# Optimization experiments

Hardware: AMD Instinct MI355X
Metric: run time of the kernel (lower is better)

## Reference

```python
import jax, jax.numpy as jnp
import numpy as np
from jax import lax

EPS = 1e-5

def _layernorm(x, g, b):
    m = x.mean(-1, keepdims=True)
    v = ((x - m) ** 2).mean(-1, keepdims=True)
    return (x - m) * lax.rsqrt(v + EPS) * g + b

def _batchnorm(x, g, b):
    # x: [N, C, L]; training-mode batch statistics (torch BatchNorm1d default)
    m = x.mean((0, 2), keepdims=True)
    v = ((x - m) ** 2).mean((0, 2), keepdims=True)
    return (x - m) * lax.rsqrt(v + EPS) * g[None, :, None] + b[None, :, None]

def _conv1d(x, w, bias, stride):
    y = lax.conv_general_dilated(x, w, window_strides=(stride,), padding='VALID',
                                 dimension_numbers=('NCH', 'OIH', 'NCH'))
    return y + bias[None, :, None]

def setup_inputs() -> dict:
    key = jax.random.key(0)
    ks = jax.random.split(key, 22)
    B, C, L = 512, 12, 5000
    NF, HID, LAT = 32, 64, 32
    def w(k, shape, fan_in):
        return jax.random.normal(k, shape, jnp.float32) * (1.0 / np.sqrt(fan_in))
    return {
        'x': jax.random.normal(ks[0], (B, C, L), jnp.float32),
        'c1w': w(ks[1], (32, C, 50), C * 50), 'c1b': jnp.zeros((32,), jnp.float32),
        'bn1g': jnp.ones((32,), jnp.float32), 'bn1b': jnp.zeros((32,), jnp.float32),
        'c2w': w(ks[2], (NF, 32, 25), 32 * 25), 'c2b': jnp.zeros((NF,), jnp.float32),
        'bn2g': jnp.ones((NF,), jnp.float32), 'bn2b': jnp.zeros((NF,), jnp.float32),
        'Wi': w(ks[3], (LAT, NF), NF) * 0.5, 'bi': jnp.zeros((LAT,), jnp.float32),
        'ln1g': jnp.ones((LAT,), jnp.float32), 'ln1b': jnp.zeros((LAT,), jnp.float32),
        'Wh': w(ks[4], (HID, LAT), LAT) * 0.5, 'bh': jnp.zeros((HID,), jnp.float32),
        'ln2g': jnp.ones((HID,), jnp.float32), 'ln2b': jnp.zeros((HID,), jnp.float32),
        'Wr': w(ks[5], (LAT, HID), HID) * 0.5, 'br': jnp.zeros((LAT,), jnp.float32),
        'Wo': w(ks[6], (LAT, LAT), LAT), 'bo': jnp.zeros((LAT,), jnp.float32),
    }

def reference(x, c1w, c1b, bn1g, bn1b, c2w, c2b, bn2g, bn2b,
              Wi, bi, ln1g, ln1b, Wh, bh, ln2g, ln2b, Wr, br, Wo, bo):
    # CNN front-end: [B,12,5000] -> [B,32,496] -> [B,32,95]
    h = jax.nn.relu(_batchnorm(_conv1d(x, c1w, c1b, 10), bn1g, bn1b))
    h = jax.nn.relu(_batchnorm(_conv1d(h, c2w, c2b, 5), bn2g, bn2b))
    feats = h.transpose(2, 0, 1)  # [T, B, NF]
    # input_proj + ln1 have no dependence on the recurrent state -> hoist out of loop
    xt_all = _layernorm(jnp.einsum('tbf,lf->tbl', feats, Wi) + bi, ln1g, ln1b)  # [T,B,LAT]

    def step(hstate, xt):
        combined = xt + hstate
        hp = jax.nn.relu(combined @ Wh.T + bh)      # [B, HID]
        hp = _layernorm(hp, ln2g, ln2b)
        hnew = jnp.tanh(hp @ Wr.T + br)             # [B, LAT]
        return hnew, hnew

    h0 = jnp.zeros((x.shape[0], Wr.shape[0]), x.dtype)
    _, outs = lax.scan(step, h0, xt_all)            # outs: [T, B, LAT]
    pooled = outs.mean(0)                           # mean over time
    return pooled @ Wo.T + bo                       # [B, LAT]
```

## Files before the change

kernel.cpp:

```cpp
#include <hip/hip_runtime.h>

#define EPS 1e-5f

#define B    512
#define C_IN 12
#define L_IN 5000
#define C1   32
#define L1   496
#define NF   32
#define L2   95
#define LAT  32
#define HID  64
#define T    L2

typedef short s16x8 __attribute__((ext_vector_type(8)));
typedef float f32x16 __attribute__((ext_vector_type(16)));

__device__ __forceinline__ ushort f2bf(float f) {
    uint u = __builtin_bit_cast(uint, f);
    u += 0x7fff + ((u >> 16) & 1);
    return (ushort)(u >> 16);
}
__device__ __forceinline__ float bf2f(ushort h) {
    return __builtin_bit_cast(float, (uint)h << 16);
}
__device__ __forceinline__ uint pk(float f) {
    ushort h = f2bf(f);
    return (uint)h | ((uint)f2bf(f - bf2f(h)) << 16);
}
__device__ __forceinline__ uint4 pack4(float4 d) {
    return make_uint4(pk(d.x), pk(d.y), pk(d.z), pk(d.w));
}

__global__ void k_prep_w(const float* __restrict__ c1w, const float* __restrict__ c2w,
                         ushort* __restrict__ wfrag1, ushort* __restrict__ wfrag2) {
    int i = blockIdx.x * 256 + threadIdx.x;
    if (i < 6144) {
        int lane = i & 63, r = i >> 6;
        int split = r & 1, s = (r >> 1) & 3, c = r >> 3;
        int oc = lane & 31, kbase = s * 16 + (lane >> 5) * 8;
        ushort o8[8];
#pragma unroll
        for (int j = 0; j < 8; ++j) {
            int kk = kbase + j;
            float w = (kk < 50) ? c1w[oc * 600 + c * 50 + kk] : 0.f;
            ushort hb = f2bf(w);
            o8[j] = split ? f2bf(w - bf2f(hb)) : hb;
        }
        ushort4* dst = reinterpret_cast<ushort4*>(wfrag1) + (size_t)i * 2;
        dst[0] = make_ushort4(o8[0], o8[1], o8[2], o8[3]);
        dst[1] = make_ushort4(o8[4], o8[5], o8[6], o8[7]);
    } else if (i < 14336) {
        int j = i - 6144;
        int lane = j & 63, r = j >> 6;
        int split = r & 1, ks = (r >> 1) & 1, c = r >> 2;
        int oc = lane & 31, kbase = ks * 16 + (lane >> 5) * 8;
        ushort o8[8];
#pragma unroll
        for (int jj = 0; jj < 8; ++jj) {
            int kk = kbase + jj;
            float w = (kk < 25) ? c2w[oc * 800 + c * 25 + kk] : 0.f;
            ushort hb = f2bf(w);
            o8[jj] = split ? f2bf(w - bf2f(hb)) : hb;
        }
        ushort4* dst = reinterpret_cast<ushort4*>(wfrag2) + (size_t)j * 2;
        dst[0] = make_ushort4(o8[0], o8[1], o8[2], o8[3]);
        dst[1] = make_ushort4(o8[4], o8[5], o8[6], o8[7]);
    }
}

__device__ __forceinline__ void conv1_compute(const uint (*xs)[1344], const uint4* wf4,
                                              int c0, int abase, int lane,
                                              f32x16& hh, f32x16& hl, f32x16& lh) {
    for (int cc = 0; cc < 6; ++cc) {
        const int c = c0 + cc;
        const uint* xc = xs[c];
        const uint4* wfc = wf4 + (size_t)c * 512 + lane;
#pragma unroll
        for (int s = 0; s < 4; ++s) {
            const int idx = abase + s * 16;
            uint2 p0 = *reinterpret_cast<const uint2*>(&xc[idx]);
            uint2 p1 = *reinterpret_cast<const uint2*>(&xc[idx + 2]);
            uint2 p2 = *reinterpret_cast<const uint2*>(&xc[idx + 4]);
            uint2 p3 = *reinterpret_cast<const uint2*>(&xc[idx + 6]);
            union { s16x8 v; uint u[4]; } ah, al, bh, bl;
            ah.u[0] = __builtin_amdgcn_perm(p0.y, p0.x, 0x05040100u);
            al.u[0] = __builtin_amdgcn_perm(p0.y, p0.x, 0x07060302u);
            ah.u[1] = __builtin_amdgcn_perm(p1.y, p1.x, 0x05040100u);
            al.u[1] = __builtin_amdgcn_perm(p1.y, p1.x, 0x07060302u);
            ah.u[2] = __builtin_amdgcn_perm(p2.y, p2.x, 0x05040100u);
            al.u[2] = __builtin_amdgcn_perm(p2.y, p2.x, 0x07060302u);
            ah.u[3] = __builtin_amdgcn_perm(p3.y, p3.x, 0x05040100u);
            al.u[3] = __builtin_amdgcn_perm(p3.y, p3.x, 0x07060302u);
            uint4 bq = wfc[s * 128];
            uint4 lq = wfc[s * 128 + 64];
            bh.u[0] = bq.x; bh.u[1] = bq.y; bh.u[2] = bq.z; bh.u[3] = bq.w;
            bl.u[0] = lq.x; bl.u[1] = lq.y; bl.u[2] = lq.z; bl.u[3] = lq.w;
            hh = __builtin_amdgcn_mfma_f32_32x32x16_bf16(ah.v, bh.v, hh, 0, 0, 0);
            hl = __builtin_amdgcn_mfma_f32_32x32x16_bf16(ah.v, bl.v, hl, 0, 0, 0);
            lh = __builtin_amdgcn_mfma_f32_32x32x16_bf16(al.v, bh.v, lh, 0, 0, 0);
        }
    }
}

__global__ __launch_bounds__(512, 4) void k_conv1(const float* __restrict__ x,
                                                  const ushort* __restrict__ wfrag,
                                                  const float* __restrict__ c1b,
                                                  float* __restrict__ y1,
                                                  float* __restrict__ raw1) {
    __shared__ uint xs[C_IN][1344];
    __shared__ float redS[4][32], redQ[4][32];
    const int chunk = blockIdx.x, b = blockIdx.y, tid = threadIdx.x;
    const int t0 = chunk * 128;
    const int v4max = min(336, (5000 - 10 * t0) >> 2);
    const float4* xb4 = reinterpret_cast<const float4*>(x + (size_t)b * (C_IN * L_IN) + 10 * t0);

    uint4* xs4 = reinterpret_cast<uint4*>(&xs[0][0]);
#pragma unroll
    for (int r = 0; r < 2; ++r) {
        float4 rg[4];
#pragma unroll
        for (int i = 0; i < 4; ++i) {
            const int v = tid + (r * 4 + i) * 512;
            const int c = v / 336, i4 = v - c * 336;
            rg[i] = make_float4(0, 0, 0, 0);
            if (v < 4032 && i4 < v4max) rg[i] = xb4[c * 1250 + i4];
        }
#pragma unroll
        for (int i = 0; i < 4; ++i) {
            const int v = tid + (r * 4 + i) * 512;
            if (v < 4032) xs4[v] = pack4(rg[i]);
        }
    }
    __syncthreads();

    const int lane = tid & 63, wv = tid >> 6;
    const int g = wv >> 2;
    const int tw = wv & 3;
    const int cl = lane & 31;
    const int kgrp = lane >> 5;
    const int abase = 10 * (tw * 32 + cl) + kgrp * 8;

    f32x16 hh, hl, lh;
#pragma unroll
    for (int i = 0; i < 16; ++i) { hh[i] = 0.f; hl[i] = 0.f; lh[i] = 0.f; }
    const uint4* wf4 = reinterpret_cast<const uint4*>(wfrag);

    conv1_compute(xs, wf4, g * 6, abase, lane, hh, hl, lh);

    f32x16 tot;
#pragma unroll
    for (int i = 0; i < 16; ++i) tot[i] = hh[i] + hl[i] + lh[i];

    __syncthreads();
    float4* pr = reinterpret_cast<float4*>(&xs[0][0]);
    if (g == 1) {
#pragma unroll
        for (int i4 = 0; i4 < 4; ++i4)
            pr[tw * 256 + i4 * 64 + lane] =
                make_float4(tot[4*i4], tot[4*i4+1], tot[4*i4+2], tot[4*i4+3]);
    }
    __syncthreads();

    float sum = 0.f, sq = 0.f;
    if (g == 0) {
        const float bias = c1b[cl];
        float* yb = y1 + ((size_t)b * C1 + cl) * L1;
#pragma unroll
        for (int q = 0; q < 4; ++q) {
            float4 p = pr[tw * 256 + q * 64 + lane];
            const int trow = t0 + tw * 32 + 8 * q + 4 * kgrp;
            float4 st;
            st.x = tot[4*q+0] + p.x + bias;
            st.y = tot[4*q+1] + p.y + bias;
            st.z = tot[4*q+2] + p.z + bias;
            st.w = tot[4*q+3] + p.w + bias;
            if (trow < L1) {
                *reinterpret_cast<float4*>(yb + trow) = st;
                sum += st.x + st.y + st.z + st.w;
                sq  += st.x * st.x + st.y * st.y + st.z * st.z + st.w * st.w;
            }
        }
        sum += __shfl_xor(sum, 32);
        sq  += __shfl_xor(sq, 32);
        if (lane < 32) { redS[tw][cl] = sum; redQ[tw][cl] = sq; }
    }
    __syncthreads();
    if (tid < 64) {
        int o = tid & 31, isQ = tid >> 5;
        float v = isQ ? (redQ[0][o] + redQ[1][o] + redQ[2][o] + redQ[3][o])
                      : (redS[0][o] + redS[1][o] + redS[2][o] + redS[3][o]);
        atomicAdd(&raw1[(isQ ? 1024 : 0) + o * 16], v);
    }
}

__global__ __launch_bounds__(384, 3) void k_conv2(const float* __restrict__ y1,
                                                  const ushort* __restrict__ wfrag2,
                                                  const float* __restrict__ c2b,
                                                  const float* __restrict__ raw1,
                                                  const float* __restrict__ bn1g,
                                                  const float* __restrict__ bn1b,
                                                  float* __restrict__ y2,
                                                  float* __restrict__ raw2) {
    __shared__ uint xs[C1 * 512];
    __shared__ float fin[64];
    __shared__ float redS[3][32], redQ[3][32];
    const int b = blockIdx.x, tid = threadIdx.x;

    if (tid < 32) {
        const float cnt = 1.f / (float)(B * L1);
        float mean = raw1[tid * 16] * cnt;
        float var = raw1[1024 + tid * 16] * cnt - mean * mean;
        float sc = bn1g[tid] * rsqrtf(var + EPS);
        fin[tid] = sc;
        fin[32 + tid] = bn1b[tid] - mean * sc;
    }
    __syncthreads();

    const float4* src = reinterpret_cast<const float4*>(y1 + (size_t)b * (C1 * L1));
    for (int v = tid; v < C1 * 128; v += 384) {
        const int c = v >> 7, i4 = v & 127;
        uint4 o = make_uint4(0, 0, 0, 0);
        if (i4 < 124) {
            const float sc = fin[c], sh = fin[32 + c];
            float4 d = src[c * 124 + i4];
            float e0 = fmaxf(fmaf(d.x, sc, sh), 0.f);
            float e1 = fmaxf(fmaf(d.y, sc, sh), 0.f);
            float e2 = fmaxf(fmaf(d.z, sc, sh), 0.f);
            float e3 = fmaxf(fmaf(d.w, sc, sh), 0.f);
            o = make_uint4(pk(e0), pk(e1), pk(e2), pk(e3));
        }
        *reinterpret_cast<uint4*>(&xs[c * 512 + 4 * i4]) = o;
    }
    __syncthreads();

    const int lane = tid & 63, wv = tid / 64;
    const int g = (wv >= 3) ? 1 : 0;
    const int tw = wv - 3 * g;
    const int cl = lane & 31;
    const int kgrp = lane >> 5;
    const int tbase = 5 * (tw * 32 + cl) + kgrp * 8;

    f32x16 hh, hl, lh;
#pragma unroll
    for (int i = 0; i < 16; ++i) { hh[i] = 0.f; hl[i] = 0.f; lh[i] = 0.f; }
    const uint4* wf4 = reinterpret_cast<const uint4*>(wfrag2);

    for (int cc = 0; cc < 16; ++cc) {
        const int c = g * 16 + cc;
        const uint* xc = xs + c * 512;
        const uint4* wfc = wf4 + (size_t)c * 256 + lane;
#pragma unroll
        for (int ks = 0; ks < 2; ++ks) {
            const int idx = tbase + ks * 16;
            uint u0 = xc[idx + 0], u1 = xc[idx + 1], u2 = xc[idx + 2], u3 = xc[idx + 3];
            uint u4 = xc[idx + 4], u5 = xc[idx + 5], u6 = xc[idx + 6], u7 = xc[idx + 7];
            union { s16x8 v; uint u[4]; } ah, al, bh, bl;
            ah.u[0] = __builtin_amdgcn_perm(u1, u0, 0x05040100u);
            al.u[0] = __builtin_amdgcn_perm(u1, u0, 0x07060302u);
            ah.u[1] = __builtin_amdgcn_perm(u3, u2, 0x05040100u);
            al.u[1] = __builtin_amdgcn_perm(u3, u2, 0x07060302u);
            ah.u[2] = __builtin_amdgcn_perm(u5, u4, 0x05040100u);
            al.u[2] = __builtin_amdgcn_perm(u5, u4, 0x07060302u);
            ah.u[3] = __builtin_amdgcn_perm(u7, u6, 0x05040100u);
            al.u[3] = __builtin_amdgcn_perm(u7, u6, 0x07060302u);
            uint4 bq = wfc[ks * 128];
            uint4 lq = wfc[ks * 128 + 64];
            bh.u[0] = bq.x; bh.u[1] = bq.y; bh.u[2] = bq.z; bh.u[3] = bq.w;
            bl.u[0] = lq.x; bl.u[1] = lq.y; bl.u[2] = lq.z; bl.u[3] = lq.w;
            hh = __builtin_amdgcn_mfma_f32_32x32x16_bf16(ah.v, bh.v, hh, 0, 0, 0);
            hl = __builtin_amdgcn_mfma_f32_32x32x16_bf16(ah.v, bl.v, hl, 0, 0, 0);
            lh = __builtin_amdgcn_mfma_f32_32x32x16_bf16(al.v, bh.v, lh, 0, 0, 0);
        }
    }

    f32x16 tot;
#pragma unroll
    for (int i = 0; i < 16; ++i) tot[i] = hh[i] + hl[i] + lh[i];

    __syncthreads();
    float4* pr = reinterpret_cast<float4*>(xs);
    if (g == 1) {
#pragma unroll
        for (int q = 0; q < 4; ++q)
            pr[tw * 256 + q * 64 + lane] =
                make_float4(tot[4*q], tot[4*q+1], tot[4*q+2], tot[4*q+3]);
    }
    __syncthreads();

    float sum = 0.f, sq = 0.f;
    if (g == 0) {
        const float bias = c2b[cl];
#pragma unroll
        for (int q = 0; q < 4; ++q) {
            float4 p = pr[tw * 256 + q * 64 + lane];
            float v4[4] = { tot[4*q+0] + p.x + bias, tot[4*q+1] + p.y + bias,
                            tot[4*q+2] + p.z + bias, tot[4*q+3] + p.w + bias };
#pragma unroll
            for (int j = 0; j < 4; ++j) {
                const int t = tw * 32 + 8 * q + 4 * kgrp + j;
                if (t < L2) {
                    y2[((size_t)b * L2 + t) * NF + cl] = v4[j];
                    sum += v4[j]; sq += v4[j] * v4[j];
                }
            }
        }
        sum += __shfl_xor(sum, 32);
        sq  += __shfl_xor(sq, 32);
        if (lane < 32) { redS[tw][cl] = sum; redQ[tw][cl] = sq; }
    }
    __syncthreads();
    if (tid < 64) {
        int o = tid & 31, isQ = tid >> 5;
        float v = isQ ? (redQ[0][o] + redQ[1][o] + redQ[2][o])
                      : (redS[0][o] + redS[1][o] + redS[2][o]);
        atomicAdd(&raw2[(isQ ? 1024 : 0) + o * 16], v);
    }
}

__global__ __launch_bounds__(256) void k_proj(const float* __restrict__ y2,
                                              const float* __restrict__ raw2,
                                              const float* __restrict__ bn2g,
                                              const float* __restrict__ bn2b,
                                              const float* __restrict__ Wi,
                                              const float* __restrict__ bi,
                                              const float* __restrict__ ln1g,
                                              const float* __restrict__ ln1b,
                                              const float* __restrict__ Wh,
                                              const float* __restrict__ bh,
                                              float* __restrict__ xt2) {
    __shared__ float fin[64];
    if (threadIdx.x < 32) {
        const float cnt = 1.f / (float)(B * L2);
        float mean = raw2[threadIdx.x * 16] * cnt;
        float var = raw2[1024 + threadIdx.x * 16] * cnt - mean * mean;
        float sc = bn2g[threadIdx.x] * rsqrtf(var + EPS);
        fin[threadIdx.x] = sc;
        fin[32 + threadIdx.x] = bn2b[threadIdx.x] - mean * sc;
    }
    __syncthreads();

    const int r = blockIdx.x * 256 + threadIdx.x;
    const int b = r / 95, t = r - b * 95;

    const float4* row = reinterpret_cast<const float4*>(y2 + (size_t)r * NF);
    float u[NF];
#pragma unroll
    for (int f4 = 0; f4 < 8; ++f4) {
        float4 v = row[f4];
        u[4*f4]   = fmaxf(fmaf(v.x, fin[4*f4],   fin[32 + 4*f4]),   0.f);
        u[4*f4+1] = fmaxf(fmaf(v.y, fin[4*f4+1], fin[32 + 4*f4+1]), 0.f);
        u[4*f4+2] = fmaxf(fmaf(v.z, fin[4*f4+2], fin[32 + 4*f4+2]), 0.f);
        u[4*f4+3] = fmaxf(fmaf(v.w, fin[4*f4+3], fin[32 + 4*f4+3]), 0.f);
    }
    float xln[LAT];
    float s = 0.f, q = 0.f;
#pragma unroll
    for (int l = 0; l < LAT; ++l) {
        float a = bi[l];
#pragma unroll
        for (int f = 0; f < NF; ++f) a = fmaf(u[f], Wi[l * NF + f], a);
        xln[l] = a; s += a; q += a * a;
    }
    const float m = s * (1.f / LAT);
    const float inv = rsqrtf(q * (1.f / LAT) - m * m + EPS);
#pragma unroll
    for (int l = 0; l < LAT; ++l) xln[l] = (xln[l] - m) * inv * ln1g[l] + ln1b[l];

    float4* dst = reinterpret_cast<float4*>(xt2 + ((size_t)t * B + b) * HID);
#pragma unroll
    for (int j4 = 0; j4 < 16; ++j4) {
        float4 o4;
        float a0 = bh[4*j4], a1 = bh[4*j4+1], a2 = bh[4*j4+2], a3 = bh[4*j4+3];
#pragma unroll
        for (int l = 0; l < LAT; ++l) {
            float xl = xln[l];
            a0 = fmaf(xl, Wh[(4*j4)   * LAT + l], a0);
            a1 = fmaf(xl, Wh[(4*j4+1) * LAT + l], a1);
            a2 = fmaf(xl, Wh[(4*j4+2) * LAT + l], a2);
            a3 = fmaf(xl, Wh[(4*j4+3) * LAT + l], a3);
        }
        o4.x = a0; o4.y = a1; o4.z = a2; o4.w = a3;
        dst[j4] = o4;
    }
}

__global__ __launch_bounds__(64) void k_rnn(const float* __restrict__ xt2,
                                            const float* __restrict__ Wh,
                                            const float* __restrict__ ln2g,
                                            const float* __restrict__ ln2b,
                                            const float* __restrict__ Wr,
                                            const float* __restrict__ br,
                                            const float* __restrict__ Wo,
                                            const float* __restrict__ bo,
                                            float* __restrict__ out) {
    __shared__ __align__(16) float aS[64];
    __shared__ __align__(16) float hS[32];
    const int lane = threadIdx.x;
    const int b = blockIdx.x;
    const int l = lane & 31;

    float whv[LAT];
#pragma unroll
    for (int i = 0; i < LAT; ++i) whv[i] = Wh[lane * LAT + i];

    float wg[HID];
    float S1 = 0.f, S2 = br[l];
#pragma unroll
    for (int j = 0; j < HID; ++j) {
        float w = Wr[l * HID + j];
        wg[j] = w * ln2g[j];
        S1 += wg[j];
        S2 = fmaf(w, ln2b[j], S2);
    }

    float hfull[LAT];
#pragma unroll
    for (int i = 0; i < LAT; ++i) hfull[i] = 0.f;
    float pooled = 0.f;
    float xq = xt2[(size_t)b * HID + lane];

    for (int t = 0; t < T; ++t) {
        float xq_next = 0.f;
        if (t + 1 < T) xq_next = xt2[((size_t)(t + 1) * B + b) * HID + lane];

        float a0 = xq, a1 = 0.f, a2c = 0.f, a3c = 0.f;
#pragma unroll
        for (int i = 0; i < 8; ++i) {
            a0  = fmaf(hfull[4*i+0], whv[4*i+0], a0);
            a1  = fmaf(hfull[4*i+1], whv[4*i+1], a1);
            a2c = fmaf(hfull[4*i+2], whv[4*i+2], a2c);
            a3c = fmaf(hfull[4*i+3], whv[4*i+3], a3c);
        }
        const float a = fmaxf((a0 + a1) + (a2c + a3c), 0.f);

        aS[lane] = a;
        asm volatile("s_waitcnt lgkmcnt(0)" ::: "memory");

        float d0 = 0.f, d1 = 0.f, d2 = 0.f, d3 = 0.f;
#pragma unroll
        for (int i = 0; i < 16; ++i) {
            float4 v = reinterpret_cast<const float4*>(aS)[i];
            d0 = fmaf(v.x, wg[4*i+0], d0); d1 = fmaf(v.y, wg[4*i+1], d1);
            d2 = fmaf(v.z, wg[4*i+2], d2); d3 = fmaf(v.w, wg[4*i+3], d3);
        }
        float s = a, q = a * a;
#pragma unroll
        for (int off = 32; off >= 1; off >>= 1) { s += __shfl_xor(s, off); q += __shfl_xor(q, off); }
        const float m = s * (1.f / HID);
        const float inv = __builtin_amdgcn_rsqf(q * (1.f / HID) - m * m + EPS);
        const float dot = (d0 + d1) + (d2 + d3);
        const float a2v = fmaf(inv, dot - m * S1, S2);

        const float z = __builtin_amdgcn_exp2f(2.8853900817779268f * a2v);
        const float h = 1.f - 2.f * __builtin_amdgcn_rcpf(z + 1.f);
        pooled += h;

        if (lane < 32) hS[lane] = h;
        asm volatile("s_waitcnt lgkmcnt(0)" ::: "memory");
#pragma unroll
        for (int i = 0; i < 8; ++i) {
            float4 hv = reinterpret_cast<const float4*>(hS)[i];
            hfull[4*i] = hv.x; hfull[4*i+1] = hv.y; hfull[4*i+2] = hv.z; hfull[4*i+3] = hv.w;
        }
        xq = xq_next;
    }
    pooled *= (1.f / T);
    if (lane < 32) aS[lane] = pooled;
    asm volatile("s_waitcnt lgkmcnt(0)" ::: "memory");

    float wov[LAT];
#pragma unroll
    for (int i = 0; i < LAT; ++i) wov[i] = Wo[l * LAT + i];
    float b0 = bo[l], b1 = 0.f, b2 = 0.f, b3 = 0.f;
#pragma unroll
    for (int i = 0; i < 8; ++i) {
        float4 pv = reinterpret_cast<const float4*>(aS)[i];
        b0 = fmaf(pv.x, wov[4*i+0], b0); b1 = fmaf(pv.y, wov[4*i+1], b1);
        b2 = fmaf(pv.z, wov[4*i+2], b2); b3 = fmaf(pv.w, wov[4*i+3], b3);
    }
    if (lane < 32) out[(size_t)b * LAT + l] = (b0 + b1) + (b2 + b3);
}

extern "C" void kernel_launch(void* const* d_in, const int* in_sizes, int n_in,
                              void* d_out, int out_size, void* d_ws, size_t ws_size,
                              hipStream_t stream) {
    const float* x    = (const float*)d_in[0];
    const float* c1w  = (const float*)d_in[1];
    const float* c1b  = (const float*)d_in[2];
    const float* bn1g = (const float*)d_in[3];
    const float* bn1b = (const float*)d_in[4];
    const float* c2w  = (const float*)d_in[5];
    const float* c2b  = (const float*)d_in[6];
    const float* bn2g = (const float*)d_in[7];
    const float* bn2b = (const float*)d_in[8];
    const float* Wi   = (const float*)d_in[9];
    const float* bi   = (const float*)d_in[10];
    const float* ln1g = (const float*)d_in[11];
    const float* ln1b = (const float*)d_in[12];
    const float* Wh   = (const float*)d_in[13];
    const float* bh   = (const float*)d_in[14];
    const float* ln2g = (const float*)d_in[15];
    const float* ln2b = (const float*)d_in[16];
    const float* Wr   = (const float*)d_in[17];
    const float* br   = (const float*)d_in[18];
    const float* Wo   = (const float*)d_in[19];
    const float* bo   = (const float*)d_in[20];

    float* ws = (float*)d_ws;
    float* raw1 = ws;
    float* raw2 = ws + 2048;
    ushort* wfrag1 = (ushort*)(ws + 4096);
    ushort* wfrag2 = (ushort*)(ws + 28672);
    float* y1   = ws + 61440;
    float* y2   = ws + 8187904;
    float* xt2  = y1;
    float* out  = (float*)d_out;

    hipMemsetAsync(raw1, 0, 4096 * sizeof(float), stream);
    k_prep_w<<<56, 256, 0, stream>>>(c1w, c2w, wfrag1, wfrag2);
    k_conv1<<<dim3(4, B), 512, 0, stream>>>(x, wfrag1, c1b, y1, raw1);
    k_conv2<<<B, 384, 0, stream>>>(y1, wfrag2, c2b, raw1, bn1g, bn1b, y2, raw2);
    k_proj<<<190, 256, 0, stream>>>(y2, raw2, bn2g, bn2b, Wi, bi, ln1g, ln1b, Wh, bh, xt2);
    k_rnn<<<B, 64, 0, stream>>>(xt2, Wh, ln2g, ln2b, Wr, br, Wo, bo, out);
}
```

Before: 229.6 us.

## Replace BN statistic atomics with per-block partials and a reduction kernel

Conv1 and conv2 now write per-block channel sum and sum-of-squares partials to workspace instead of atomically adding into shared counters. Two new single-block kernels reduce those partials and compute the batchnorm scale and shift once, and the downstream kernels just load the finished values. This drops the memset and the atomic contention on a few addresses. In exchange it adds two small kernel launches, and each one runs on a single workgroup.

```diff
diff --git a/kernel.cpp b/kernel.cpp
--- a/kernel.cpp
+++ b/kernel.cpp
@@ -66,6 +66,34 @@
         ushort4* dst = reinterpret_cast<ushort4*>(wfrag2) + (size_t)j * 2;
         dst[0] = make_ushort4(o8[0], o8[1], o8[2], o8[3]);
         dst[1] = make_ushort4(o8[4], o8[5], o8[6], o8[7]);
+    }
+}
+
+__global__ __launch_bounds__(1024) void k_bnred(const float* __restrict__ part, int nblk,
+                                                const float* __restrict__ g,
+                                                const float* __restrict__ bb,
+                                                float count, float* __restrict__ fin) {
+    __shared__ float lds[16 * 64];
+    const int t = threadIdx.x;
+    const int o = t & 63, seg = t >> 6;
+    const int per = nblk >> 4;
+    float s = 0.f;
+    const float* p = part + (size_t)seg * per * 64 + o;
+    for (int i = 0; i < per; ++i) s += p[(size_t)i * 64];
+    lds[seg * 64 + o] = s;
+    __syncthreads();
+    if (t < 32) {
+        float sum = 0.f, sq = 0.f;
+#pragma unroll
+        for (int sg = 0; sg < 16; ++sg) {
+            sum += lds[sg * 64 + t];
+            sq  += lds[sg * 64 + t + 32];
+        }
+        const float mean = sum / count;
+        const float var = sq / count - mean * mean;
+        const float sc = g[t] * rsqrtf(var + EPS);
+        fin[t] = sc;
+        fin[32 + t] = bb[t] - mean * sc;
     }
 }
 
@@ -107,7 +135,7 @@
                                                   const ushort* __restrict__ wfrag,
                                                   const float* __restrict__ c1b,
                                                   float* __restrict__ y1,
-                                                  float* __restrict__ raw1) {
+                                                  float* __restrict__ raw1p) {
     __shared__ uint xs[C_IN][1344];
     __shared__ float redS[4][32], redQ[4][32];
     const int chunk = blockIdx.x, b = blockIdx.y, tid = threadIdx.x;
@@ -190,31 +218,22 @@
         int o = tid & 31, isQ = tid >> 5;
         float v = isQ ? (redQ[0][o] + redQ[1][o] + redQ[2][o] + redQ[3][o])
                       : (redS[0][o] + redS[1][o] + redS[2][o] + redS[3][o]);
-        atomicAdd(&raw1[(isQ ? 1024 : 0) + o * 16], v);
+        raw1p[(size_t)(b * 4 + chunk) * 64 + tid] = v;
     }
 }
 
 __global__ __launch_bounds__(384, 3) void k_conv2(const float* __restrict__ y1,
                                                   const ushort* __restrict__ wfrag2,
                                                   const float* __restrict__ c2b,
-                                                  const float* __restrict__ raw1,
-                                                  const float* __restrict__ bn1g,
-                                                  const float* __restrict__ bn1b,
+                                                  const float* __restrict__ fin1,
                                                   float* __restrict__ y2,
-                                                  float* __restrict__ raw2) {
+                                                  float* __restrict__ raw2p) {
     __shared__ uint xs[C1 * 512];
     __shared__ float fin[64];
     __shared__ float redS[3][32], redQ[3][32];
     const int b = blockIdx.x, tid = threadIdx.x;
 
-    if (tid < 32) {
-        const float cnt = 1.f / (float)(B * L1);
-        float mean = raw1[tid * 16] * cnt;
-        float var = raw1[1024 + tid * 16] * cnt - mean * mean;
-        float sc = bn1g[tid] * rsqrtf(var + EPS);
-        fin[tid] = sc;
-        fin[32 + tid] = bn1b[tid] - mean * sc;
-    }
+    if (tid < 64) fin[tid] = fin1[tid];
     __syncthreads();
 
     const float4* src = reinterpret_cast<const float4*>(y1 + (size_t)b * (C1 * L1));
@@ -314,14 +333,12 @@
         int o = tid & 31, isQ = tid >> 5;
         float v = isQ ? (redQ[0][o] + redQ[1][o] + redQ[2][o])
                       : (redS[0][o] + redS[1][o] + redS[2][o]);
-        atomicAdd(&raw2[(isQ ? 1024 : 0) + o * 16], v);
+        raw2p[(size_t)b * 64 + tid] = v;
     }
 }
 
 __global__ __launch_bounds__(256) void k_proj(const float* __restrict__ y2,
-                                              const float* __restrict__ raw2,
-                                              const float* __restrict__ bn2g,
-                                              const float* __restrict__ bn2b,
+                                              const float* __restrict__ fin2g,
                                               const float* __restrict__ Wi,
                                               const float* __restrict__ bi,
                                               const float* __restrict__ ln1g,
@@ -330,14 +347,7 @@
                                               const float* __restrict__ bh,
                                               float* __restrict__ xt2) {
     __shared__ float fin[64];
-    if (threadIdx.x < 32) {
-        const float cnt = 1.f / (float)(B * L2);
-        float mean = raw2[threadIdx.x * 16] * cnt;
-        float var = raw2[1024 + threadIdx.x * 16] * cnt - mean * mean;
-        float sc = bn2g[threadIdx.x] * rsqrtf(var + EPS);
-        fin[threadIdx.x] = sc;
-        fin[32 + threadIdx.x] = bn2b[threadIdx.x] - mean * sc;
-    }
+    if (threadIdx.x < 64) fin[threadIdx.x] = fin2g[threadIdx.x];
     __syncthreads();
 
     const int r = blockIdx.x * 256 + threadIdx.x;
@@ -508,19 +518,22 @@
     const float* bo   = (const float*)d_in[20];
 
     float* ws = (float*)d_ws;
-    float* raw1 = ws;
-    float* raw2 = ws + 2048;
+    float* fin1 = ws;
+    float* fin2 = ws + 64;
     ushort* wfrag1 = (ushort*)(ws + 4096);
     ushort* wfrag2 = (ushort*)(ws + 28672);
     float* y1   = ws + 61440;
     float* y2   = ws + 8187904;
+    float* raw1p = y2;
+    float* raw2p = ws + 9744384;
     float* xt2  = y1;
     float* out  = (float*)d_out;
 
-    hipMemsetAsync(raw1, 0, 4096 * sizeof(float), stream);
     k_prep_w<<<56, 256, 0, stream>>>(c1w, c2w, wfrag1, wfrag2);
-    k_conv1<<<dim3(4, B), 512, 0, stream>>>(x, wfrag1, c1b, y1, raw1);
-    k_conv2<<<B, 384, 0, stream>>>(y1, wfrag2, c2b, raw1, bn1g, bn1b, y2, raw2);
-    k_proj<<<190, 256, 0, stream>>>(y2, raw2, bn2g, bn2b, Wi, bi, ln1g, ln1b, Wh, bh, xt2);
+    k_conv1<<<dim3(4, B), 512, 0, stream>>>(x, wfrag1, c1b, y1, raw1p);
+    k_bnred<<<1, 1024, 0, stream>>>(raw1p, 2048, bn1g, bn1b, (float)(B * L1), fin1);
+    k_conv2<<<B, 384, 0, stream>>>(y1, wfrag2, c2b, fin1, y2, raw2p);
+    k_bnred<<<1, 1024, 0, stream>>>(raw2p, 512, bn2g, bn2b, (float)(B * L2), fin2);
+    k_proj<<<190, 256, 0, stream>>>(y2, fin2, Wi, bi, ln1g, ln1b, Wh, bh, xt2);
     k_rnn<<<B, 64, 0, stream>>>(xt2, Wh, ln2g, ln2b, Wr, br, Wo, bo, out);
 }
```

After: 241.2 us. 5.1% more time.
